# Performance work log

Hardware: AMD Instinct MI355X
Metric: run time of the kernel (lower is better)

The kernel has to match this reference:

```python
import jax, jax.numpy as jnp
import numpy as np

B, L, DH = 16, 8192, 256
T, DG = 512, 512
DP = 256  # d_proj


def setup_inputs() -> dict:
    key = jax.random.key(0)
    k1, k2, k3, k4, k5 = jax.random.split(key, 5)
    H = jax.random.normal(k1, (B, L, DH), dtype=jnp.float32)
    G = jax.random.normal(k2, (B, T, DG), dtype=jnp.float32)
    mask = jax.random.randint(k3, (B, L), 0, 2).astype(bool)
    # nn.Linear(bias=False) weights: (out_features, in_features)
    Wk = jax.random.normal(k4, (DP, DH), dtype=jnp.float32) * (DH ** -0.5)
    Wq = jax.random.normal(k5, (DP, DG), dtype=jnp.float32) * (DG ** -0.5)
    return {"H": H, "G": G, "mask": mask, "Wk": Wk, "Wq": Wq}


def reference(H, G, mask, Wk, Wq):
    scale = DP ** -0.5
    K = jnp.einsum('bld,pd->blp', H, Wk)           # (B, L, P)
    Q = jnp.einsum('btg,pg->btp', G, Wq)           # (B, T, P)
    logits = jnp.einsum('btp,blp->btl', Q, K) * scale  # (B, T, L)
    logits = jnp.where(mask[:, None, :], -jnp.inf, logits)
    alpha = jax.nn.softmax(logits, axis=-1)        # dropout=0 -> identity
    Z = jnp.einsum('btl,bld->btd', alpha, H)       # (B, T, Dh)
    return Z
```

## Files before the change

### kernel.cpp

```cpp
#include <hip/hip_runtime.h>
#include <hip/hip_bf16.h>
#include <math.h>

#define B_  16
#define L_  8192
#define DH_ 256
#define T_  512
#define DG_ 512
#define DP_ 256

typedef __attribute__((ext_vector_type(8))) short short8b;
typedef __attribute__((ext_vector_type(4))) short short4b;
typedef __attribute__((ext_vector_type(4))) float f32x4;

typedef const __attribute__((address_space(1))) void gas_t;
typedef __attribute__((address_space(3))) void las_t;
typedef __attribute__((address_space(3))) short lds_short;
#define GLOAD_LDS16(g, l) __builtin_amdgcn_global_load_lds((gas_t*)(g), (las_t*)(l), 16, 0, 0)

#define TRR(dst, P, OFF) \
    asm volatile("ds_read_b64_tr_b16 %0, %1 offset:%c2" : "=v"(dst) : "v"(P), "i"(OFF))

__device__ int g_cnt[B_];
__device__ int g_dst[B_][L_];

static __device__ __forceinline__ short f2bf(float f) {
    union { __hip_bfloat16 b; short s; } u;
    u.b = __float2bfloat16(f);
    return u.s;
}

static __device__ __forceinline__ float bf2f(short s) {
    union { float f; unsigned u; } v;
    v.u = ((unsigned)(unsigned short)s) << 16;
    return v.f;
}

static __device__ __forceinline__ unsigned cvtpk_bf16(float lo, float hi) {
    unsigned r;
    asm("v_cvt_pk_bf16_f32 %0, %1, %2" : "=v"(r) : "v"(lo), "v"(hi));
    return r;
}

static __device__ __forceinline__ float exp2_raw(float x) {
    float r;
    asm("v_exp_f32 %0, %1" : "=v"(r) : "v"(x));
    return r;
}

static __device__ __forceinline__ short8b cvt8(const float* __restrict__ src) {
    float4 a = *(const float4*)src;
    float4 b = *(const float4*)(src + 4);
    short8b o;
    o[0] = f2bf(a.x); o[1] = f2bf(a.y); o[2] = f2bf(a.z); o[3] = f2bf(a.w);
    o[4] = f2bf(b.x); o[5] = f2bf(b.y); o[6] = f2bf(b.z); o[7] = f2bf(b.w);
    return o;
}

__global__ __launch_bounds__(1024) void prep_all(const int* __restrict__ mask,
                                                 const float* __restrict__ Wk,
                                                 const float* __restrict__ Wq,
                                                 short* __restrict__ Wktf,
                                                 short* __restrict__ Wqf,
                                                 float alpha_q) {
    const int blk = blockIdx.x;
    const int tid = threadIdx.x, lane = tid & 63;
    const int l15 = lane & 15, g = lane >> 4;

    if (blk < 16) {
        const int b = blk, wid = tid >> 6;
        __shared__ int wsum[16];
        const int* mb = mask + (size_t)b * L_;
        int base = 0;
        for (int it = 0; it < L_ / 1024; ++it) {
            const int l = it * 1024 + tid;
            const int um = (mb[l] == 0);
            unsigned long long bal = __ballot(um);
            const int below = __popcll(bal & ((1ull << lane) - 1ull));
            const int wtot  = __popcll(bal);
            if (lane == 0) wsum[wid] = wtot;
            __syncthreads();
            int wbase = 0, tot = 0;
#pragma unroll
            for (int w = 0; w < 16; ++w) {
                wbase += (w < wid) ? wsum[w] : 0;
                tot   += wsum[w];
            }
            if (um) g_dst[b][l] = base + wbase + below;
            base += tot;
            __syncthreads();
        }
        if (tid == 0) g_cnt[b] = base;
    } else if (blk < 24) {
        const int f = (blk - 16) * 16 + (tid >> 6);
        const int nf = f >> 3, ks = f & 7;
        short8b o;
#pragma unroll
        for (int j = 0; j < 8; ++j)
            o[j] = f2bf(Wk[(size_t)(ks * 32 + g * 8 + j) * DH_ + nf * 16 + l15]);
        *(short8b*)&Wktf[(size_t)f * 512 + lane * 8] = o;
    } else {
        const int f = (blk - 24) * 16 + (tid >> 6);
        const int nf = f >> 4, ks = f & 15;
        const float* src = Wq + (size_t)(nf * 16 + l15) * DG_ + ks * 32 + g * 8;
        short8b o;
#pragma unroll
        for (int j = 0; j < 8; ++j) o[j] = f2bf(src[j] * alpha_q);
        *(short8b*)&Wqf[(size_t)f * 512 + lane * 8] = o;
    }
}

__global__ __launch_bounds__(256) void produce_all(const float* __restrict__ G,
                                                   const short* __restrict__ Wqf,
                                                   const short* __restrict__ Wktf,
                                                   short* __restrict__ Qc,
                                                   const float* __restrict__ H,
                                                   const int* __restrict__ mask,
                                                   short* __restrict__ Hsb) {
    __shared__ short sL[16896];

    const int blk = blockIdx.x;
    const int tid = threadIdx.x;

    if (blk < 128) {
        const int wid = tid >> 6, lane = tid & 63;
        const int l15 = lane & 15, g = lane >> 4;
        const size_t m0 = (size_t)blk * 64;

        const float* arow = G + (m0 + wid * 16 + l15) * DG_;
        short8b af[16];
#pragma unroll
        for (int ks = 0; ks < 16; ++ks) {
            float4 a = *(const float4*)&arow[ks * 32 + g * 8];
            float4 c = *(const float4*)&arow[ks * 32 + g * 8 + 4];
            short8b o;
            o[0] = f2bf(a.x); o[1] = f2bf(a.y); o[2] = f2bf(a.z); o[3] = f2bf(a.w);
            o[4] = f2bf(c.x); o[5] = f2bf(c.y); o[6] = f2bf(c.z); o[7] = f2bf(c.w);
            af[ks] = o;
        }
        f32x4 acc[16];
#pragma unroll
        for (int i = 0; i < 16; ++i) acc[i] = (f32x4){0.f, 0.f, 0.f, 0.f};
#pragma unroll
        for (int ks = 0; ks < 16; ++ks)
#pragma unroll
            for (int nf = 0; nf < 16; ++nf) {
                short8b wf = *(const short8b*)&Wqf[(size_t)(nf * 16 + ks) * 512 + lane * 8];
                acc[nf] = __builtin_amdgcn_mfma_f32_16x16x32_bf16(af[ks], wf, acc[nf], 0, 0, 0);
            }
#pragma unroll
        for (int nf = 0; nf < 16; ++nf)
#pragma unroll
            for (int r = 0; r < 4; ++r)
                sL[(wid * 16 + 4 * g + r) * 264 + nf * 16 + l15] = f2bf(acc[nf][r]);
        __syncthreads();

        short8b af2[8];
#pragma unroll
        for (int ks = 0; ks < 8; ++ks)
            af2[ks] = *(const short8b*)&sL[(wid * 16 + l15) * 264 + ks * 32 + g * 8];
        f32x4 acc2[16];
#pragma unroll
        for (int i = 0; i < 16; ++i) acc2[i] = (f32x4){0.f, 0.f, 0.f, 0.f};
#pragma unroll
        for (int ks = 0; ks < 8; ++ks)
#pragma unroll
            for (int nf = 0; nf < 16; ++nf) {
                short8b wf = *(const short8b*)&Wktf[(size_t)(nf * 8 + ks) * 512 + lane * 8];
                acc2[nf] = __builtin_amdgcn_mfma_f32_16x16x32_bf16(af2[ks], wf, acc2[nf], 0, 0, 0);
            }
#pragma unroll
        for (int nf = 0; nf < 16; ++nf)
#pragma unroll
            for (int r = 0; r < 4; ++r)
                Qc[(m0 + wid * 16 + 4 * g + r) * DP_ + nf * 16 + l15] = f2bf(acc2[nf][r]);
    } else {
        const int gb = blk - 128;
        const int b  = gb >> 7;
        const int c0 = (gb & 127) * 64;
        const int r = tid >> 2, sub = tid & 3;
        const int l = c0 + r;

        if (mask[(size_t)b * L_ + l] != 0) return;

        const int dld = g_dst[b][l];
        const int dl  = dld & 63;
        short* dtile = Hsb + (size_t)b * (L_ * DH_) + (size_t)(dld >> 6) * 16384
                     + (dl >> 2) * 1024 + (dl & 3) * 16;
        const float* src = H + ((size_t)b * L_ + l) * DH_;
#pragma unroll
        for (int j = 0; j < 8; ++j) {
            const int c = j * 4 + sub;
            short8b o = cvt8(&src[c * 8]);
            *(short8b*)&dtile[(c >> 1) * 64 + (c & 1) * 8] = o;
        }
    }
}

template <int LSPLIT>
__global__ __launch_bounds__(256, 2) void attn_pipe5(const short* __restrict__ Hsb,
                                                     const short* __restrict__ Qb,
                                                     float* __restrict__ Zdirect,
                                                     short* __restrict__ Zp,
                                                     float* __restrict__ Sp) {
    constexpr int LSB = (LSPLIT == 8) ? 3 : (LSPLIT == 4) ? 2 : (LSPLIT == 2) ? 1 : 0;

    __shared__ short sbuf[2][16384];

    const int wg   = blockIdx.x;
    const int low  = wg & 7;
    const int rest = wg >> 3;
    const int tg   = rest & 3;
    const int ghi  = rest >> 2;
    const int grp  = ghi * 8 + low;
    const int b    = grp >> LSB;
    const int lq   = grp & (LSPLIT - 1);

    const int tid  = threadIdx.x;
    const int wid  = tid >> 6;
    const int lane = tid & 63;
    const int l15  = lane & 15, g = lane >> 4;
    const int th   = wid;
    const int t0   = tg * 128;

    const int cnt      = g_cnt[b];
    const int nt_total = (cnt + 63) >> 6;
    const int q        = (nt_total + LSPLIT - 1) >> LSB;
    const int start    = lq * q;
    int ntiles = nt_total - start;
    ntiles = ntiles < 0 ? 0 : (ntiles > q ? q : ntiles);

    const short* Hb = Hsb + (size_t)b * (L_ * DH_);

    short8b qf[2][8];
#pragma unroll
    for (int nt = 0; nt < 2; ++nt) {
        const short* qrow = Qb + ((size_t)b * T_ + t0 + th * 32 + nt * 16 + l15) * DP_;
#pragma unroll
        for (int ks = 0; ks < 8; ++ks)
            qf[nt][ks] = *(const short8b*)&qrow[ks * 32 + g * 8];
    }

    f32x4 zacc[2][16];
#pragma unroll
    for (int nt = 0; nt < 2; ++nt)
#pragma unroll
        for (int nf = 0; nf < 16; ++nf)
            zacc[nt][nf] = (f32x4){0.f, 0.f, 0.f, 0.f};
    float s_part[2] = {0.f, 0.f};

    const int  idx0  = (l15 + 32 * (g & 1)) * 4;
    const int  idx1  = idx0 + 64;
    const bool ltsel = (g >> 1) != 0;

    lds_short* trb0 = (lds_short*)&sbuf[0][0] + (lane >> 4) * 2048 + (lane & 15) * 4;
    lds_short* trb1 = (lds_short*)&sbuf[1][0] + (lane >> 4) * 2048 + (lane & 15) * 4;

    auto STAGE = [&](int bi, int gi) {
        const int gic = gi < 127 ? gi : 127;
        const short* src = Hb + (size_t)gic * 16384;
#pragma unroll
        for (int c = 0; c < 8; ++c) {
            const int u = wid * 512 + c * 64 + lane;
            GLOAD_LDS16(src + u * 8, &sbuf[bi][u * 8]);
        }
    };

    if (ntiles > 0) {
        STAGE(0, start);
        asm volatile("s_waitcnt vmcnt(0)" ::: "memory");
        __builtin_amdgcn_s_barrier();
        STAGE(1, start + 1);

        for (int i = 0; i < ntiles; ++i) {
            const int cur = i & 1;
            const short* sK = &sbuf[cur][0];
            const int gi = start + i;
            const int limit = cnt - (gi << 6);

            unsigned pk[4][2][2];
#pragma unroll
            for (int lh2 = 0; lh2 < 2; ++lh2) {
                f32x4 sv[2][2];
#pragma unroll
                for (int ltl = 0; ltl < 2; ++ltl)
#pragma unroll
                    for (int nt = 0; nt < 2; ++nt)
                        sv[ltl][nt] = (f32x4){0.f, 0.f, 0.f, 0.f};
                __builtin_amdgcn_s_setprio(1);
#pragma unroll
                for (int ltl = 0; ltl < 2; ++ltl) {
                    const int lt = lh2 * 2 + ltl;
#pragma unroll
                    for (int ks = 0; ks < 8; ++ks) {
                        short8b af = *(const short8b*)&sK[(lt * 4 + (l15 >> 2)) * 1024 +
                                                          (ks * 2 + (g >> 1)) * 64 +
                                                          (l15 & 3) * 16 + (g & 1) * 8];
                        sv[ltl][0] = __builtin_amdgcn_mfma_f32_16x16x32_bf16(af, qf[0][ks], sv[ltl][0], 0, 0, 0);
                        sv[ltl][1] = __builtin_amdgcn_mfma_f32_16x16x32_bf16(af, qf[1][ks], sv[ltl][1], 0, 0, 0);
                    }
                }
                __builtin_amdgcn_s_setprio(0);

                if (limit >= 64) {
#pragma unroll
                    for (int ltl = 0; ltl < 2; ++ltl)
#pragma unroll
                        for (int nt = 0; nt < 2; ++nt) {
                            float p0 = exp2_raw(sv[ltl][nt][0]);
                            float p1 = exp2_raw(sv[ltl][nt][1]);
                            float p2 = exp2_raw(sv[ltl][nt][2]);
                            float p3 = exp2_raw(sv[ltl][nt][3]);
                            s_part[nt] += (p0 + p1) + (p2 + p3);
                            pk[lh2 * 2 + ltl][nt][0] = cvtpk_bf16(p0, p1);
                            pk[lh2 * 2 + ltl][nt][1] = cvtpk_bf16(p2, p3);
                        }
                } else {
#pragma unroll
                    for (int ltl = 0; ltl < 2; ++ltl) {
                        const int lt = lh2 * 2 + ltl;
                        const int thr = limit - lt * 16 - 4 * g;
                        float madd[4];
#pragma unroll
                        for (int r = 0; r < 4; ++r) madd[r] = (r < thr) ? 0.f : -INFINITY;
#pragma unroll
                        for (int nt = 0; nt < 2; ++nt) {
                            float p0 = exp2_raw(sv[ltl][nt][0] + madd[0]);
                            float p1 = exp2_raw(sv[ltl][nt][1] + madd[1]);
                            float p2 = exp2_raw(sv[ltl][nt][2] + madd[2]);
                            float p3 = exp2_raw(sv[ltl][nt][3] + madd[3]);
                            s_part[nt] += (p0 + p1) + (p2 + p3);
                            pk[lt][nt][0] = cvtpk_bf16(p0, p1);
                            pk[lt][nt][1] = cvtpk_bf16(p2, p3);
                        }
                    }
                }
            }

            short8b pa[2][2];
#pragma unroll
            for (int h = 0; h < 2; ++h)
#pragma unroll
                for (int nt = 0; nt < 2; ++nt) {
                    int A0 = __builtin_amdgcn_ds_bpermute(idx0, (int)pk[2 * h][nt][0]);
                    int A1 = __builtin_amdgcn_ds_bpermute(idx0, (int)pk[2 * h][nt][1]);
                    int B0 = __builtin_amdgcn_ds_bpermute(idx0, (int)pk[2 * h + 1][nt][0]);
                    int B1 = __builtin_amdgcn_ds_bpermute(idx0, (int)pk[2 * h + 1][nt][1]);
                    int C0 = __builtin_amdgcn_ds_bpermute(idx1, (int)pk[2 * h][nt][0]);
                    int C1 = __builtin_amdgcn_ds_bpermute(idx1, (int)pk[2 * h][nt][1]);
                    int D0 = __builtin_amdgcn_ds_bpermute(idx1, (int)pk[2 * h + 1][nt][0]);
                    int D1 = __builtin_amdgcn_ds_bpermute(idx1, (int)pk[2 * h + 1][nt][1]);
                    union { int d[4]; short8b v; } u;
                    u.d[0] = ltsel ? B0 : A0;
                    u.d[1] = ltsel ? B1 : A1;
                    u.d[2] = ltsel ? D0 : C0;
                    u.d[3] = ltsel ? D1 : C1;
                    pa[h][nt] = u.v;
                }

            lds_short* ptr = cur ? trb1 : trb0;
            short4b tb[2][4];
            TRR(tb[0][0], ptr, 0 * 2048);
            TRR(tb[0][1], ptr, 1 * 2048);
            TRR(tb[0][2], ptr, 8 * 2048);
            TRR(tb[0][3], ptr, 9 * 2048);
            __builtin_amdgcn_s_setprio(1);
#pragma unroll
            for (int nf = 0; nf < 16; ++nf) {
                if (nf < 15) {
                    TRR(tb[(nf + 1) & 1][0], ptr, 0 * 2048 + (nf + 1) * 128);
                    TRR(tb[(nf + 1) & 1][1], ptr, 1 * 2048 + (nf + 1) * 128);
                    TRR(tb[(nf + 1) & 1][2], ptr, 8 * 2048 + (nf + 1) * 128);
                    TRR(tb[(nf + 1) & 1][3], ptr, 9 * 2048 + (nf + 1) * 128);
                    asm volatile("s_waitcnt lgkmcnt(4)" ::: "memory");
                } else {
                    asm volatile("s_waitcnt lgkmcnt(0)" ::: "memory");
                }
                __builtin_amdgcn_sched_barrier(0);
#pragma unroll
                for (int h = 0; h < 2; ++h) {
                    short8b hb = __builtin_shufflevector(tb[nf & 1][2 * h], tb[nf & 1][2 * h + 1],
                                                         0, 1, 2, 3, 4, 5, 6, 7);
                    zacc[0][nf] = __builtin_amdgcn_mfma_f32_16x16x32_bf16(pa[h][0], hb, zacc[0][nf], 0, 0, 0);
                    zacc[1][nf] = __builtin_amdgcn_mfma_f32_16x16x32_bf16(pa[h][1], hb, zacc[1][nf], 0, 0, 0);
                }
            }
            __builtin_amdgcn_s_setprio(0);

            asm volatile("s_waitcnt vmcnt(0)" ::: "memory");
            __builtin_amdgcn_s_barrier();
            if (i + 2 < ntiles) STAGE(cur, gi + 2);
        }
    }

    float sful[2];
#pragma unroll
    for (int nt = 0; nt < 2; ++nt) {
        float v = s_part[nt];
        v += __shfl_xor(v, 16, 64);
        v += __shfl_xor(v, 32, 64);
        sful[nt] = v;
    }

    if constexpr (LSPLIT == 1) {
#pragma unroll
        for (int nt = 0; nt < 2; ++nt)
#pragma unroll
            for (int r = 0; r < 4; ++r) {
                float s = __shfl(sful[nt], 4 * g + r, 64);
                float ri = (s > 0.f) ? 1.f / s : 0.f;
                float* zrow = Zdirect + ((size_t)b * T_ + t0 + th * 32 + nt * 16 + 4 * g + r) * DH_;
#pragma unroll
                for (int nf = 0; nf < 16; ++nf)
                    zrow[nf * 16 + l15] = zacc[nt][nf][r] * ri;
            }
    } else {
        const int pb = (b * 4 + tg) * LSPLIT + lq;
        if (lane < 16) {
            Sp[(size_t)pb * 128 + th * 32 + l15]      = sful[0];
            Sp[(size_t)pb * 128 + th * 32 + 16 + l15] = sful[1];
        }
#pragma unroll
        for (int nt = 0; nt < 2; ++nt)
#pragma unroll
            for (int r = 0; r < 4; ++r) {
                short* zrow = Zp + ((size_t)pb * 128 + th * 32 + nt * 16 + 4 * g + r) * DH_;
#pragma unroll
                for (int nf = 0; nf < 16; ++nf)
                    zrow[nf * 16 + l15] = f2bf(zacc[nt][nf][r]);
            }
    }
}

template <int LSPLIT>
__global__ __launch_bounds__(256) void combine_z(const short* __restrict__ Zp,
                                                 const float* __restrict__ Sp,
                                                 float* __restrict__ Z) {
    const int idx8 = blockIdx.x * 256 + threadIdx.x;
    const int d0 = (idx8 & 31) * 8;
    const int t  = (idx8 >> 5) & 511;
    const int b  = idx8 >> 14;
    const int tg = t >> 7, tl = t & 127;
    const size_t pb0 = (size_t)(b * 4 + tg) * LSPLIT;

    float acc[8] = {0.f, 0.f, 0.f, 0.f, 0.f, 0.f, 0.f, 0.f};
    float s = 0.f;
#pragma unroll
    for (int lq = 0; lq < LSPLIT; ++lq) {
        short8b v = *(const short8b*)&Zp[((pb0 + lq) * 128 + tl) * 256 + d0];
#pragma unroll
        for (int j = 0; j < 8; ++j) acc[j] += bf2f(v[j]);
        s += Sp[(pb0 + lq) * 128 + tl];
    }
    const float ri = (s > 0.f) ? 1.f / s : 0.f;
    float* zrow = Z + (((size_t)b * T_ + t) * DH_ + d0);
    *(float4*)zrow       = make_float4(acc[0] * ri, acc[1] * ri, acc[2] * ri, acc[3] * ri);
    *(float4*)(zrow + 4) = make_float4(acc[4] * ri, acc[5] * ri, acc[6] * ri, acc[7] * ri);
}

extern "C" void kernel_launch(void* const* d_in, const int* in_sizes, int n_in,
                              void* d_out, int out_size, void* d_ws, size_t ws_size,
                              hipStream_t stream) {
    const float* H    = (const float*)d_in[0];
    const float* G    = (const float*)d_in[1];
    const int*   mask = (const int*)d_in[2];
    const float* Wk   = (const float*)d_in[3];
    const float* Wq   = (const float*)d_in[4];
    float* Z = (float*)d_out;

    short* Wktf = (short*)d_ws;
    short* Wqf  = Wktf + 65536ull;
    short* Hsb  = Wqf + 131072ull;
    short* Qc   = Hsb + 33554432ull;
    short* Htc  = Qc + 2097152ull;
    short* Zpb  = Htc + 33554432ull;

    const float alpha_q = 1.4426950408889634f / 16.0f;

    prep_all<<<dim3(40), 1024, 0, stream>>>(mask, Wk, Wq, Wktf, Wqf, alpha_q);
    produce_all<<<dim3(128 + B_ * 128), 256, 0, stream>>>(G, Wqf, Wktf, Qc, H, mask, Hsb);

    const size_t base = 138805248ull;
    if (ws_size >= base + 8388608ull * 8 + 262144ull) {
        float* Sp = (float*)(Zpb + (size_t)64 * 8 * 128 * 256);
        attn_pipe5<8><<<dim3(512), 256, 0, stream>>>(Hsb, Qc, Z, Zpb, Sp);
        combine_z<8><<<dim3(1024), 256, 0, stream>>>(Zpb, Sp, Z);
    } else if (ws_size >= base + 8388608ull * 4 + 131072ull) {
        float* Sp = (float*)(Zpb + (size_t)64 * 4 * 128 * 256);
        attn_pipe5<4><<<dim3(256), 256, 0, stream>>>(Hsb, Qc, Z, Zpb, Sp);
        combine_z<4><<<dim3(1024), 256, 0, stream>>>(Zpb, Sp, Z);
    } else if (ws_size >= base + 8388608ull * 2 + 65536ull) {
        float* Sp = (float*)(Zpb + (size_t)64 * 2 * 128 * 256);
        attn_pipe5<2><<<dim3(128), 256, 0, stream>>>(Hsb, Qc, Z, Zpb, Sp);
        combine_z<2><<<dim3(1024), 256, 0, stream>>>(Zpb, Sp, Z);
    } else {
        attn_pipe5<1><<<dim3(64), 256, 0, stream>>>(Hsb, Qc, Z, Zpb, nullptr);
    }
}
```

Before: 101.1 us.

## Halve attention tile sizes to 64 queries and 32 keys, raising occupancy

The attention kernel now works on 64 query rows per workgroup (16 per wave) and 32-key tiles instead of 128 rows and 64 keys. LDS per block is halved and register state (Q fragments, Z accumulators) drops, so launch bounds ask for 3 blocks per CU and the grid doubles. The trade-off is that each K/V tile is reused by half as many queries, which doubles global/L2 traffic for H and adds more loop-iteration overhead per FLOP. The combine kernel and partial-buffer indexing are updated to the new tiling.

```diff
diff --git a/kernel.cpp b/kernel.cpp
--- a/kernel.cpp
+++ b/kernel.cpp
@@ -198,20 +198,20 @@
 }
 
 template <int LSPLIT>
-__global__ __launch_bounds__(256, 2) void attn_pipe5(const short* __restrict__ Hsb,
+__global__ __launch_bounds__(256, 3) void attn_pipe6(const short* __restrict__ Hsb,
                                                      const short* __restrict__ Qb,
                                                      float* __restrict__ Zdirect,
                                                      short* __restrict__ Zp,
                                                      float* __restrict__ Sp) {
     constexpr int LSB = (LSPLIT == 8) ? 3 : (LSPLIT == 4) ? 2 : (LSPLIT == 2) ? 1 : 0;
 
-    __shared__ short sbuf[2][16384];
+    __shared__ short sbuf[2][8192];
 
     const int wg   = blockIdx.x;
     const int low  = wg & 7;
     const int rest = wg >> 3;
-    const int tg   = rest & 3;
-    const int ghi  = rest >> 2;
+    const int tg   = rest & 7;
+    const int ghi  = rest >> 3;
     const int grp  = ghi * 8 + low;
     const int b    = grp >> LSB;
     const int lq   = grp & (LSPLIT - 1);
@@ -221,10 +221,10 @@
     const int lane = tid & 63;
     const int l15  = lane & 15, g = lane >> 4;
     const int th   = wid;
-    const int t0   = tg * 128;
+    const int t0   = tg * 64;
 
     const int cnt      = g_cnt[b];
-    const int nt_total = (cnt + 63) >> 6;
+    const int nt_total = (cnt + 31) >> 5;
     const int q        = (nt_total + LSPLIT - 1) >> LSB;
     const int start    = lq * q;
     int ntiles = nt_total - start;
@@ -232,22 +232,18 @@
 
     const short* Hb = Hsb + (size_t)b * (L_ * DH_);
 
-    short8b qf[2][8];
-#pragma unroll
-    for (int nt = 0; nt < 2; ++nt) {
-        const short* qrow = Qb + ((size_t)b * T_ + t0 + th * 32 + nt * 16 + l15) * DP_;
+    short8b qf[8];
+    {
+        const short* qrow = Qb + ((size_t)b * T_ + t0 + th * 16 + l15) * DP_;
 #pragma unroll
         for (int ks = 0; ks < 8; ++ks)
-            qf[nt][ks] = *(const short8b*)&qrow[ks * 32 + g * 8];
-    }
-
-    f32x4 zacc[2][16];
-#pragma unroll
-    for (int nt = 0; nt < 2; ++nt)
-#pragma unroll
-        for (int nf = 0; nf < 16; ++nf)
-            zacc[nt][nf] = (f32x4){0.f, 0.f, 0.f, 0.f};
-    float s_part[2] = {0.f, 0.f};
+            qf[ks] = *(const short8b*)&qrow[ks * 32 + g * 8];
+    }
+
+    f32x4 zacc[16];
+#pragma unroll
+    for (int nf = 0; nf < 16; ++nf) zacc[nf] = (f32x4){0.f, 0.f, 0.f, 0.f};
+    float s_part = 0.f;
 
     const int  idx0  = (l15 + 32 * (g & 1)) * 4;
     const int  idx1  = idx0 + 64;
@@ -257,11 +253,11 @@
     lds_short* trb1 = (lds_short*)&sbuf[1][0] + (lane >> 4) * 2048 + (lane & 15) * 4;
 
     auto STAGE = [&](int bi, int gi) {
-        const int gic = gi < 127 ? gi : 127;
-        const short* src = Hb + (size_t)gic * 16384;
-#pragma unroll
-        for (int c = 0; c < 8; ++c) {
-            const int u = wid * 512 + c * 64 + lane;
+        const int gic = gi < 255 ? gi : 255;
+        const short* src = Hb + (size_t)gic * 8192;
+#pragma unroll
+        for (int c = 0; c < 4; ++c) {
+            const int u = wid * 256 + c * 64 + lane;
             GLOAD_LDS16(src + u * 8, &sbuf[bi][u * 8]);
         }
     };
@@ -276,114 +272,89 @@
             const int cur = i & 1;
             const short* sK = &sbuf[cur][0];
             const int gi = start + i;
-            const int limit = cnt - (gi << 6);
-
-            unsigned pk[4][2][2];
-#pragma unroll
-            for (int lh2 = 0; lh2 < 2; ++lh2) {
-                f32x4 sv[2][2];
-#pragma unroll
-                for (int ltl = 0; ltl < 2; ++ltl)
-#pragma unroll
-                    for (int nt = 0; nt < 2; ++nt)
-                        sv[ltl][nt] = (f32x4){0.f, 0.f, 0.f, 0.f};
-                __builtin_amdgcn_s_setprio(1);
-#pragma unroll
-                for (int ltl = 0; ltl < 2; ++ltl) {
-                    const int lt = lh2 * 2 + ltl;
-#pragma unroll
-                    for (int ks = 0; ks < 8; ++ks) {
-                        short8b af = *(const short8b*)&sK[(lt * 4 + (l15 >> 2)) * 1024 +
-                                                          (ks * 2 + (g >> 1)) * 64 +
-                                                          (l15 & 3) * 16 + (g & 1) * 8];
-                        sv[ltl][0] = __builtin_amdgcn_mfma_f32_16x16x32_bf16(af, qf[0][ks], sv[ltl][0], 0, 0, 0);
-                        sv[ltl][1] = __builtin_amdgcn_mfma_f32_16x16x32_bf16(af, qf[1][ks], sv[ltl][1], 0, 0, 0);
-                    }
+            const int limit = cnt - (gi << 5);
+
+            f32x4 sv[2];
+            sv[0] = (f32x4){0.f, 0.f, 0.f, 0.f};
+            sv[1] = (f32x4){0.f, 0.f, 0.f, 0.f};
+            __builtin_amdgcn_s_setprio(1);
+#pragma unroll
+            for (int lt = 0; lt < 2; ++lt) {
+#pragma unroll
+                for (int ks = 0; ks < 8; ++ks) {
+                    short8b af = *(const short8b*)&sK[(lt * 4 + (l15 >> 2)) * 1024 +
+                                                      (ks * 2 + (g >> 1)) * 64 +
+                                                      (l15 & 3) * 16 + (g & 1) * 8];
+                    sv[lt] = __builtin_amdgcn_mfma_f32_16x16x32_bf16(af, qf[ks], sv[lt], 0, 0, 0);
                 }
-                __builtin_amdgcn_s_setprio(0);
-
-                if (limit >= 64) {
-#pragma unroll
-                    for (int ltl = 0; ltl < 2; ++ltl)
-#pragma unroll
-                        for (int nt = 0; nt < 2; ++nt) {
-                            float p0 = exp2_raw(sv[ltl][nt][0]);
-                            float p1 = exp2_raw(sv[ltl][nt][1]);
-                            float p2 = exp2_raw(sv[ltl][nt][2]);
-                            float p3 = exp2_raw(sv[ltl][nt][3]);
-                            s_part[nt] += (p0 + p1) + (p2 + p3);
-                            pk[lh2 * 2 + ltl][nt][0] = cvtpk_bf16(p0, p1);
-                            pk[lh2 * 2 + ltl][nt][1] = cvtpk_bf16(p2, p3);
-                        }
-                } else {
-#pragma unroll
-                    for (int ltl = 0; ltl < 2; ++ltl) {
-                        const int lt = lh2 * 2 + ltl;
-                        const int thr = limit - lt * 16 - 4 * g;
-                        float madd[4];
-#pragma unroll
-                        for (int r = 0; r < 4; ++r) madd[r] = (r < thr) ? 0.f : -INFINITY;
-#pragma unroll
-                        for (int nt = 0; nt < 2; ++nt) {
-                            float p0 = exp2_raw(sv[ltl][nt][0] + madd[0]);
-                            float p1 = exp2_raw(sv[ltl][nt][1] + madd[1]);
-                            float p2 = exp2_raw(sv[ltl][nt][2] + madd[2]);
-                            float p3 = exp2_raw(sv[ltl][nt][3] + madd[3]);
-                            s_part[nt] += (p0 + p1) + (p2 + p3);
-                            pk[lt][nt][0] = cvtpk_bf16(p0, p1);
-                            pk[lt][nt][1] = cvtpk_bf16(p2, p3);
-                        }
-                    }
+            }
+            __builtin_amdgcn_s_setprio(0);
+
+            unsigned pk[2][2];
+            if (limit >= 32) {
+#pragma unroll
+                for (int lt = 0; lt < 2; ++lt) {
+                    float p0 = exp2_raw(sv[lt][0]);
+                    float p1 = exp2_raw(sv[lt][1]);
+                    float p2 = exp2_raw(sv[lt][2]);
+                    float p3 = exp2_raw(sv[lt][3]);
+                    s_part += (p0 + p1) + (p2 + p3);
+                    pk[lt][0] = cvtpk_bf16(p0, p1);
+                    pk[lt][1] = cvtpk_bf16(p2, p3);
                 }
-            }
-
-            short8b pa[2][2];
-#pragma unroll
-            for (int h = 0; h < 2; ++h)
-#pragma unroll
-                for (int nt = 0; nt < 2; ++nt) {
-                    int A0 = __builtin_amdgcn_ds_bpermute(idx0, (int)pk[2 * h][nt][0]);
-                    int A1 = __builtin_amdgcn_ds_bpermute(idx0, (int)pk[2 * h][nt][1]);
-                    int B0 = __builtin_amdgcn_ds_bpermute(idx0, (int)pk[2 * h + 1][nt][0]);
-                    int B1 = __builtin_amdgcn_ds_bpermute(idx0, (int)pk[2 * h + 1][nt][1]);
-                    int C0 = __builtin_amdgcn_ds_bpermute(idx1, (int)pk[2 * h][nt][0]);
-                    int C1 = __builtin_amdgcn_ds_bpermute(idx1, (int)pk[2 * h][nt][1]);
-                    int D0 = __builtin_amdgcn_ds_bpermute(idx1, (int)pk[2 * h + 1][nt][0]);
-                    int D1 = __builtin_amdgcn_ds_bpermute(idx1, (int)pk[2 * h + 1][nt][1]);
-                    union { int d[4]; short8b v; } u;
-                    u.d[0] = ltsel ? B0 : A0;
-                    u.d[1] = ltsel ? B1 : A1;
-                    u.d[2] = ltsel ? D0 : C0;
-                    u.d[3] = ltsel ? D1 : C1;
-                    pa[h][nt] = u.v;
+            } else {
+#pragma unroll
+                for (int lt = 0; lt < 2; ++lt) {
+                    const int thr = limit - lt * 16 - 4 * g;
+                    float madd[4];
+#pragma unroll
+                    for (int r = 0; r < 4; ++r) madd[r] = (r < thr) ? 0.f : -INFINITY;
+                    float p0 = exp2_raw(sv[lt][0] + madd[0]);
+                    float p1 = exp2_raw(sv[lt][1] + madd[1]);
+                    float p2 = exp2_raw(sv[lt][2] + madd[2]);
+                    float p3 = exp2_raw(sv[lt][3] + madd[3]);
+                    s_part += (p0 + p1) + (p2 + p3);
+                    pk[lt][0] = cvtpk_bf16(p0, p1);
+                    pk[lt][1] = cvtpk_bf16(p2, p3);
                 }
+            }
+
+            short8b pa;
+            {
+                int A0 = __builtin_amdgcn_ds_bpermute(idx0, (int)pk[0][0]);
+                int A1 = __builtin_amdgcn_ds_bpermute(idx0, (int)pk[0][1]);
+                int B0 = __builtin_amdgcn_ds_bpermute(idx0, (int)pk[1][0]);
+                int B1 = __builtin_amdgcn_ds_bpermute(idx0, (int)pk[1][1]);
+                int C0 = __builtin_amdgcn_ds_bpermute(idx1, (int)pk[0][0]);
+                int C1 = __builtin_amdgcn_ds_bpermute(idx1, (int)pk[0][1]);
+                int D0 = __builtin_amdgcn_ds_bpermute(idx1, (int)pk[1][0]);
+                int D1 = __builtin_amdgcn_ds_bpermute(idx1, (int)pk[1][1]);
+                union { int d[4]; short8b v; } u;
+                u.d[0] = ltsel ? B0 : A0;
+                u.d[1] = ltsel ? B1 : A1;
+                u.d[2] = ltsel ? D0 : C0;
+                u.d[3] = ltsel ? D1 : C1;
+                pa = u.v;
+            }
 
             lds_short* ptr = cur ? trb1 : trb0;
-            short4b tb[2][4];
-            TRR(tb[0][0], ptr, 0 * 2048);
-            TRR(tb[0][1], ptr, 1 * 2048);
-            TRR(tb[0][2], ptr, 8 * 2048);
-            TRR(tb[0][3], ptr, 9 * 2048);
+            short4b tb[2][2];
+            TRR(tb[0][0], ptr, 0);
+            TRR(tb[0][1], ptr, 2048);
             __builtin_amdgcn_s_setprio(1);
 #pragma unroll
             for (int nf = 0; nf < 16; ++nf) {
                 if (nf < 15) {
-                    TRR(tb[(nf + 1) & 1][0], ptr, 0 * 2048 + (nf + 1) * 128);
-                    TRR(tb[(nf + 1) & 1][1], ptr, 1 * 2048 + (nf + 1) * 128);
-                    TRR(tb[(nf + 1) & 1][2], ptr, 8 * 2048 + (nf + 1) * 128);
-                    TRR(tb[(nf + 1) & 1][3], ptr, 9 * 2048 + (nf + 1) * 128);
-                    asm volatile("s_waitcnt lgkmcnt(4)" ::: "memory");
+                    TRR(tb[(nf + 1) & 1][0], ptr, 0 + (nf + 1) * 128);
+                    TRR(tb[(nf + 1) & 1][1], ptr, 2048 + (nf + 1) * 128);
+                    asm volatile("s_waitcnt lgkmcnt(2)" ::: "memory");
                 } else {
                     asm volatile("s_waitcnt lgkmcnt(0)" ::: "memory");
                 }
                 __builtin_amdgcn_sched_barrier(0);
-#pragma unroll
-                for (int h = 0; h < 2; ++h) {
-                    short8b hb = __builtin_shufflevector(tb[nf & 1][2 * h], tb[nf & 1][2 * h + 1],
-                                                         0, 1, 2, 3, 4, 5, 6, 7);
-                    zacc[0][nf] = __builtin_amdgcn_mfma_f32_16x16x32_bf16(pa[h][0], hb, zacc[0][nf], 0, 0, 0);
-                    zacc[1][nf] = __builtin_amdgcn_mfma_f32_16x16x32_bf16(pa[h][1], hb, zacc[1][nf], 0, 0, 0);
-                }
+                short8b hb = __builtin_shufflevector(tb[nf & 1][0], tb[nf & 1][1],
+                                                     0, 1, 2, 3, 4, 5, 6, 7);
+                zacc[nf] = __builtin_amdgcn_mfma_f32_16x16x32_bf16(pa, hb, zacc[nf], 0, 0, 0);
             }
             __builtin_amdgcn_s_setprio(0);
 
@@ -393,42 +364,35 @@
         }
     }
 
-    float sful[2];
-#pragma unroll
-    for (int nt = 0; nt < 2; ++nt) {
-        float v = s_part[nt];
+    float sful;
+    {
+        float v = s_part;
         v += __shfl_xor(v, 16, 64);
         v += __shfl_xor(v, 32, 64);
-        sful[nt] = v;
+        sful = v;
     }
 
     if constexpr (LSPLIT == 1) {
 #pragma unroll
-        for (int nt = 0; nt < 2; ++nt)
-#pragma unroll
-            for (int r = 0; r < 4; ++r) {
-                float s = __shfl(sful[nt], 4 * g + r, 64);
-                float ri = (s > 0.f) ? 1.f / s : 0.f;
-                float* zrow = Zdirect + ((size_t)b * T_ + t0 + th * 32 + nt * 16 + 4 * g + r) * DH_;
-#pragma unroll
-                for (int nf = 0; nf < 16; ++nf)
-                    zrow[nf * 16 + l15] = zacc[nt][nf][r] * ri;
-            }
+        for (int r = 0; r < 4; ++r) {
+            float s = __shfl(sful, 4 * g + r, 64);
+            float ri = (s > 0.f) ? 1.f / s : 0.f;
+            float* zrow = Zdirect + ((size_t)b * T_ + t0 + th * 16 + 4 * g + r) * DH_;
+#pragma unroll
+            for (int nf = 0; nf < 16; ++nf)
+                zrow[nf * 16 + l15] = zacc[nf][r] * ri;
+        }
     } else {
-        const int pb = (b * 4 + tg) * LSPLIT + lq;
-        if (lane < 16) {
-            Sp[(size_t)pb * 128 + th * 32 + l15]      = sful[0];
-            Sp[(size_t)pb * 128 + th * 32 + 16 + l15] = sful[1];
-        }
-#pragma unroll
-        for (int nt = 0; nt < 2; ++nt)
-#pragma unroll
-            for (int r = 0; r < 4; ++r) {
-                short* zrow = Zp + ((size_t)pb * 128 + th * 32 + nt * 16 + 4 * g + r) * DH_;
-#pragma unroll
-                for (int nf = 0; nf < 16; ++nf)
-                    zrow[nf * 16 + l15] = f2bf(zacc[nt][nf][r]);
-            }
+        const int pb = (b * 8 + tg) * LSPLIT + lq;
+        if (lane < 16)
+            Sp[(size_t)pb * 64 + th * 16 + l15] = sful;
+#pragma unroll
+        for (int r = 0; r < 4; ++r) {
+            short* zrow = Zp + ((size_t)pb * 64 + th * 16 + 4 * g + r) * DH_;
+#pragma unroll
+            for (int nf = 0; nf < 16; ++nf)
+                zrow[nf * 16 + l15] = f2bf(zacc[nf][r]);
+        }
     }
 }
 
@@ -440,17 +404,17 @@
     const int d0 = (idx8 & 31) * 8;
     const int t  = (idx8 >> 5) & 511;
     const int b  = idx8 >> 14;
-    const int tg = t >> 7, tl = t & 127;
-    const size_t pb0 = (size_t)(b * 4 + tg) * LSPLIT;
+    const int tg = t >> 6, tl = t & 63;
+    const size_t pb0 = (size_t)(b * 8 + tg) * LSPLIT;
 
     float acc[8] = {0.f, 0.f, 0.f, 0.f, 0.f, 0.f, 0.f, 0.f};
     float s = 0.f;
 #pragma unroll
     for (int lq = 0; lq < LSPLIT; ++lq) {
-        short8b v = *(const short8b*)&Zp[((pb0 + lq) * 128 + tl) * 256 + d0];
+        short8b v = *(const short8b*)&Zp[((pb0 + lq) * 64 + tl) * 256 + d0];
 #pragma unroll
         for (int j = 0; j < 8; ++j) acc[j] += bf2f(v[j]);
-        s += Sp[(pb0 + lq) * 128 + tl];
+        s += Sp[(pb0 + lq) * 64 + tl];
     }
     const float ri = (s > 0.f) ? 1.f / s : 0.f;
     float* zrow = Z + (((size_t)b * T_ + t) * DH_ + d0);
@@ -482,18 +446,18 @@
 
     const size_t base = 138805248ull;
     if (ws_size >= base + 8388608ull * 8 + 262144ull) {
-        float* Sp = (float*)(Zpb + (size_t)64 * 8 * 128 * 256);
-        attn_pipe5<8><<<dim3(512), 256, 0, stream>>>(Hsb, Qc, Z, Zpb, Sp);
+        float* Sp = (float*)(Zpb + 2097152ull * 8);
+        attn_pipe6<8><<<dim3(1024), 256, 0, stream>>>(Hsb, Qc, Z, Zpb, Sp);
         combine_z<8><<<dim3(1024), 256, 0, stream>>>(Zpb, Sp, Z);
     } else if (ws_size >= base + 8388608ull * 4 + 131072ull) {
-        float* Sp = (float*)(Zpb + (size_t)64 * 4 * 128 * 256);
-        attn_pipe5<4><<<dim3(256), 256, 0, stream>>>(Hsb, Qc, Z, Zpb, Sp);
+        float* Sp = (float*)(Zpb + 2097152ull * 4);
+        attn_pipe6<4><<<dim3(512), 256, 0, stream>>>(Hsb, Qc, Z, Zpb, Sp);
         combine_z<4><<<dim3(1024), 256, 0, stream>>>(Zpb, Sp, Z);
     } else if (ws_size >= base + 8388608ull * 2 + 65536ull) {
-        float* Sp = (float*)(Zpb + (size_t)64 * 2 * 128 * 256);
-        attn_pipe5<2><<<dim3(128), 256, 0, stream>>>(Hsb, Qc, Z, Zpb, Sp);
+        float* Sp = (float*)(Zpb + 2097152ull * 2);
+        attn_pipe6<2><<<dim3(256), 256, 0, stream>>>(Hsb, Qc, Z, Zpb, Sp);
         combine_z<2><<<dim3(1024), 256, 0, stream>>>(Zpb, Sp, Z);
     } else {
-        attn_pipe5<1><<<dim3(64), 256, 0, stream>>>(Hsb, Qc, Z, Zpb, nullptr);
-    }
-}
+        attn_pipe6<1><<<dim3(128), 256, 0, stream>>>(Hsb, Qc, Z, Zpb, nullptr);
+    }
+}
```

New measurement: 113.9 us. 1.13x slower.
